# Optimization experiments

Hardware: AMD Instinct MI355X
Metric: run time of the kernel (lower is better)

The kernel has to match this reference:

```python
import jax, jax.numpy as jnp
import numpy as np

EPS = 1e-5

def _act_quant(x):
    # per-token int8 absmax quantization (BitNet b1.58)
    scale = 127.0 / jnp.clip(jnp.max(jnp.abs(x), axis=-1, keepdims=True), EPS)
    return jnp.clip(jnp.round(x * scale), -128.0, 127.0) / scale

def _weight_quant(w):
    # per-tensor ternary quantization: round(w/mean|w|) clipped to {-1,0,1}
    scale = 1.0 / jnp.clip(jnp.mean(jnp.abs(w)), EPS)
    return jnp.clip(jnp.round(w * scale), -1.0, 1.0) / scale

def _ste(x, q):
    # straight-through estimator: forward uses q, backward passes through x
    return x + jax.lax.stop_gradient(q - x)

def bitlinear(x, w):
    xq = _ste(x, _act_quant(x))
    wq = _ste(w, _weight_quant(w))
    return jnp.einsum('btd,hd->bth', xq, wq)

def setup_inputs() -> dict:
    key = jax.random.key(0)
    k1, k2, k3 = jax.random.split(key, 3)
    B, T, D, H = 4, 1024, 2048, 8192
    x = jax.random.normal(k1, (B, T, D), dtype=jnp.float32)
    w1 = jax.random.normal(k2, (H, D), dtype=jnp.float32) * 0.02
    w2 = jax.random.normal(k3, (D, H), dtype=jnp.float32) * 0.02
    return {"x": x, "w1": w1, "w2": w2}

def reference(x, w1, w2):
    h = jax.nn.relu(bitlinear(x, w1))   # [B, T, H]
    out = bitlinear(h, w2)              # [B, T, D]
    return out
```

## Files before the change

### kernel.cpp

```cpp
#include <hip/hip_runtime.h>
#include <hip/hip_bf16.h>

#define EPSF 1e-5f

typedef int v4i __attribute__((ext_vector_type(4)));
typedef short v8s __attribute__((ext_vector_type(8)));

static constexpr int BB = 4, TT = 1024, DD = 2048, HH = 8192;
static constexpr int MROWS = BB * TT;
static constexpr long long WCOUNT = (long long)DD * HH;


__device__ __forceinline__ void async_copy16(const void* g, void* l) {
  __builtin_amdgcn_global_load_lds(
      (const __attribute__((address_space(1))) unsigned int*)g,
      (__attribute__((address_space(3))) unsigned int*)l,
      16, 0, 0);
}

__device__ __forceinline__ int pack4(float a, float b, float c, float d,
                                     float scale, float lo, float hi) {
  int ia = (int)fminf(fmaxf(rintf(a * scale), lo), hi);
  int ib = (int)fminf(fmaxf(rintf(b * scale), lo), hi);
  int ic = (int)fminf(fmaxf(rintf(c * scale), lo), hi);
  int id = (int)fminf(fmaxf(rintf(d * scale), lo), hi);
  return (ia & 0xff) | ((ib & 0xff) << 8) | ((ic & 0xff) << 16) | ((id & 0xff) << 24);
}

__device__ __forceinline__ float abs4(float4 v) {
  return fmaxf(fmaxf(fabsf(v.x), fabsf(v.y)), fmaxf(fabsf(v.z), fabsf(v.w)));
}

__device__ __forceinline__ int blockMaxI256(int v) {
  #pragma unroll
  for (int off = 32; off; off >>= 1) v = max(v, __shfl_down(v, off, 64));
  __shared__ int sm[4];
  int lane = threadIdx.x & 63, wv = threadIdx.x >> 6;
  if (lane == 0) sm[wv] = v;
  __syncthreads();
  return max(max(sm[0], sm[1]), max(sm[2], sm[3]));
}

__device__ __forceinline__ void swizzle_tiles(int& mt, int& nt) {
  int Mt = gridDim.y, Nt = gridDim.x;
  int id = blockIdx.y * Nt + blockIdx.x;
  int c = id & 7, k = id >> 3;
  int pm = (Mt >= Nt) ? 4 : 2;
  int PM = Mt / pm, PN = Nt / (8 / pm);
  int pr = c % pm, pc = c / pm;
  mt = pr * PM + (k % PM);
  nt = pc * PN + (k / PM);
}


__global__ __launch_bounds__(256) void abs_sum_kernel(
    const float* __restrict__ w1, const float* __restrict__ w2,
    float* __restrict__ partials) {
  const int y = blockIdx.y, bid = blockIdx.x, t = threadIdx.x;
  const int lane = t & 63, wv = t >> 6;
  const float4* w4 = (const float4*)(y ? w2 : w1);
  const long long base = (long long)bid * 2048;
  float4 u[8];
  #pragma unroll
  for (int k = 0; k < 8; k++) u[k] = w4[base + t + k * 256];
  float s = 0.f;
  #pragma unroll
  for (int k = 0; k < 8; k++)
    s += fabsf(u[k].x) + fabsf(u[k].y) + fabsf(u[k].z) + fabsf(u[k].w);
  #pragma unroll
  for (int off = 32; off; off >>= 1) s += __shfl_down(s, off, 64);
  __shared__ float sm[4];
  if (lane == 0) sm[wv] = s;
  __syncthreads();
  if (t == 0) partials[y * 2048 + bid] = sm[0] + sm[1] + sm[2] + sm[3];
}


__global__ __launch_bounds__(256) void quant_w_kernel(
    const float* __restrict__ w1, const float* __restrict__ w2,
    const float* __restrict__ partials, float* __restrict__ meanw,
    signed char* __restrict__ q1, signed char* __restrict__ q2) {
  const int y = blockIdx.y, bid = blockIdx.x, t = threadIdx.x;
  const int lane = t & 63, wv = t >> 6;

  double d = 0.0;
  #pragma unroll
  for (int j = 0; j < 8; j++) d += (double)partials[y * 2048 + t + j * 256];
  #pragma unroll
  for (int off = 32; off; off >>= 1) d += __shfl_down(d, off, 64);
  __shared__ double smd[4];
  if (lane == 0) smd[wv] = d;
  __syncthreads();
  double sum = smd[0] + smd[1] + smd[2] + smd[3];
  float mean = fmaxf((float)(sum * (1.0 / (double)WCOUNT)), EPSF);
  if (bid == 0 && t == 0) meanw[y] = mean;
  float sc = 1.0f / mean;

  const float4* w4 = (const float4*)(y ? w2 : w1);
  int* q4 = (int*)(y ? q2 : q1);
  const long long base = (long long)bid * 2048;
  float4 u[8];
  #pragma unroll
  for (int k = 0; k < 8; k++) u[k] = w4[base + t + k * 256];
  #pragma unroll
  for (int k = 0; k < 8; k++)
    q4[base + t + k * 256] = pack4(u[k].x, u[k].y, u[k].z, u[k].w, sc, -1.f, 1.f);
}


__global__ __launch_bounds__(256) void quant_x_kernel(
    const float* __restrict__ x, signed char* __restrict__ xq,
    float* __restrict__ ascale) {
  int lane = threadIdx.x & 63, wv = threadIdx.x >> 6;
  int row = blockIdx.x * 4 + wv;
  const float4* xr = (const float4*)(x + (size_t)row * DD);
  float4 v[8];
  #pragma unroll
  for (int j = 0; j < 8; j++) v[j] = xr[lane + j * 64];
  float m = 0.f;
  #pragma unroll
  for (int j = 0; j < 8; j++) m = fmaxf(m, abs4(v[j]));
  #pragma unroll
  for (int off = 32; off; off >>= 1) m = fmaxf(m, __shfl_down(m, off, 64));
  m = __shfl(m, 0, 64);
  float am = fmaxf(m, EPSF);
  float scale = 127.0f / am;
  int* out = (int*)(xq + (size_t)row * DD);
  #pragma unroll
  for (int j = 0; j < 8; j++)
    out[lane + j * 64] = pack4(v[j].x, v[j].y, v[j].z, v[j].w, scale, -128.f, 127.f);
  if (lane == 0) ascale[row] = am / 127.0f;
}


__global__ __launch_bounds__(256) void quant_h_kernel(
    const short* __restrict__ h, signed char* __restrict__ hq,
    float* __restrict__ a2, const float* __restrict__ a1,
    const float* __restrict__ meanw) {
  int row = blockIdx.x;
  int t = threadIdx.x;
  const v8s* hr = (const v8s*)(h + (size_t)row * HH);
  v8s v[4];
  #pragma unroll
  for (int i = 0; i < 4; i++) v[i] = hr[t + i * 256];
  int mx = 0;
  #pragma unroll
  for (int i = 0; i < 4; i++)
    #pragma unroll
    for (int j = 0; j < 8; j++) mx = max(mx, (int)v[i][j]);
  int bmx = blockMaxI256(mx);
  float f = a1[row] * meanw[0];
  float maxh = (float)bmx * f;
  float am = fmaxf(maxh, EPSF);
  float scale = 127.0f / am;
  int* out = (int*)(hq + (size_t)row * HH);
  #pragma unroll
  for (int i = 0; i < 4; i++) {
    out[(t + i * 256) * 2] =
        pack4((float)v[i][0] * f, (float)v[i][1] * f, (float)v[i][2] * f,
              (float)v[i][3] * f, scale, -128.f, 127.f);
    out[(t + i * 256) * 2 + 1] =
        pack4((float)v[i][4] * f, (float)v[i][5] * f, (float)v[i][6] * f,
              (float)v[i][7] * f, scale, -128.f, 127.f);
  }
  if (t == 0) a2[row] = am / 127.0f;
}


template <int MODE, int BK>
__global__ __launch_bounds__(256) void gemm_i8_kernel(
    const signed char* __restrict__ A, const signed char* __restrict__ B,
    void* __restrict__ Cout, const float* __restrict__ ascale,
    const float* __restrict__ wmean_p, int M, int N, int K) {
  constexpr int CH = BK / 16;
  constexpr int SEGROWS = 1024 / BK;
  constexpr int SPW = BK / 32;
  __shared__ signed char As[128 * BK];
  __shared__ signed char Bs[128 * BK];

  const int t = threadIdx.x;
  const int lane = t & 63, wv = t >> 6;
  const int wm = wv >> 1, wn = wv & 1;
  int mt, nt;
  swizzle_tiles(mt, nt);
  const int m0 = mt * 128, n0 = nt * 128;
  const int q = lane >> 4;

  const signed char* aSrc[SPW];
  const signed char* bSrc[SPW];
  #pragma unroll
  for (int i = 0; i < SPW; i++) {
    int seg = wv * SPW + i;
    int r = seg * SEGROWS + lane / CH;
    int c = (lane % CH) ^ (r & (CH - 1));
    aSrc[i] = A + (size_t)(m0 + r) * K + c * 16;
    bSrc[i] = B + (size_t)(n0 + r) * K + c * 16;
  }

  v4i acc[4][4];
  #pragma unroll
  for (int i = 0; i < 4; i++)
    #pragma unroll
    for (int j = 0; j < 4; j++) {
      v4i z = {0, 0, 0, 0};
      acc[i][j] = z;
    }

  int rowA[4], rowB[4];
  #pragma unroll
  for (int i = 0; i < 4; i++) {
    rowA[i] = wm * 64 + i * 16 + (lane & 15);
    rowB[i] = wn * 64 + i * 16 + (lane & 15);
  }

  for (int k0 = 0; k0 < K; k0 += BK) {
    #pragma unroll
    for (int i = 0; i < SPW; i++) {
      async_copy16(aSrc[i] + k0, &As[(wv * SPW + i) * 1024]);
      async_copy16(bSrc[i] + k0, &Bs[(wv * SPW + i) * 1024]);
    }
    __syncthreads();
    #pragma unroll
    for (int kc = 0; kc < CH / 4; kc++) {
      v4i af[4], bf[4];
      #pragma unroll
      for (int i = 0; i < 4; i++) {
        int ca = (kc * 4 + q) ^ (rowA[i] & (CH - 1));
        af[i] = *(const v4i*)(As + rowA[i] * BK + ca * 16);
        int cb = (kc * 4 + q) ^ (rowB[i] & (CH - 1));
        bf[i] = *(const v4i*)(Bs + rowB[i] * BK + cb * 16);
      }
      #pragma unroll
      for (int i = 0; i < 4; i++)
        #pragma unroll
        for (int j = 0; j < 4; j++)
          acc[i][j] = __builtin_amdgcn_mfma_i32_16x16x64_i8(af[i], bf[j], acc[i][j], 0, 0, 0);
    }
    __syncthreads();
  }

  if constexpr (MODE == 1) {
    short* C = (short*)Cout;
    #pragma unroll
    for (int i = 0; i < 4; i++) {
      int mBase = m0 + wm * 64 + i * 16 + q * 4;
      #pragma unroll
      for (int e = 0; e < 4; e++) {
        #pragma unroll
        for (int j = 0; j < 4; j++) {
          int n = n0 + wn * 64 + j * 16 + (lane & 15);
          int r = acc[i][j][e];
          r = r < 0 ? 0 : (r > 32767 ? 32767 : r);
          C[(size_t)(mBase + e) * N + n] = (short)r;
        }
      }
    }
  } else {
    float* C = (float*)Cout;
    float wmean = wmean_p[0];
    #pragma unroll
    for (int i = 0; i < 4; i++) {
      int mBase = m0 + wm * 64 + i * 16 + q * 4;
      #pragma unroll
      for (int e = 0; e < 4; e++) {
        float f = ascale[mBase + e] * wmean;
        #pragma unroll
        for (int j = 0; j < 4; j++) {
          int n = n0 + wn * 64 + j * 16 + (lane & 15);
          C[(size_t)(mBase + e) * N + n] = (float)acc[i][j][e] * f;
        }
      }
    }
  }
}


extern "C" void kernel_launch(void* const* d_in, const int* in_sizes, int n_in,
                              void* d_out, int out_size, void* d_ws, size_t ws_size,
                              hipStream_t stream) {
  const float* x  = (const float*)d_in[0];
  const float* w1 = (const float*)d_in[1];
  const float* w2 = (const float*)d_in[2];
  float* out = (float*)d_out;

  char* ws = (char*)d_ws;
  float* meanw = (float*)ws;
  float* partials = (float*)(ws + 1024);
  float* a1 = (float*)(ws + 20480);
  float* a2 = (float*)(ws + 40960);
  signed char* w1q = (signed char*)(ws + 65536);
  signed char* w2q = w1q + (size_t)WCOUNT;
  signed char* xq  = w2q + (size_t)WCOUNT;
  signed char* hq  = xq + (size_t)MROWS * DD;
  short* h16 = (short*)(hq + (size_t)MROWS * HH);

  abs_sum_kernel<<<dim3(2048, 2), 256, 0, stream>>>(w1, w2, partials);
  quant_w_kernel<<<dim3(2048, 2), 256, 0, stream>>>(w1, w2, partials, meanw, w1q, w2q);
  quant_x_kernel<<<MROWS / 4, 256, 0, stream>>>(x, xq, a1);
  gemm_i8_kernel<1, 128><<<dim3(HH / 128, MROWS / 128), 256, 0, stream>>>(
      xq, w1q, h16, nullptr, meanw, MROWS, HH, DD);
  quant_h_kernel<<<MROWS, 256, 0, stream>>>(h16, hq, a2, a1, meanw);
  gemm_i8_kernel<0, 256><<<dim3(DD / 128, MROWS / 128), 256, 0, stream>>>(
      hq, w2q, out, a2, &meanw[1], MROWS, DD, HH);
}
```

Before: 375.2 us.

## Replace int8 GEMM with 4-slot async LDS ring pipeline and larger 512-thread tiles

```diff
diff --git a/kernel.cpp b/kernel.cpp
--- a/kernel.cpp
+++ b/kernel.cpp
@@ -16,6 +16,20 @@
       (const __attribute__((address_space(1))) unsigned int*)g,
       (__attribute__((address_space(3))) unsigned int*)l,
       16, 0, 0);
+}
+
+template <int N>
+__device__ __forceinline__ void wait_bar() {
+  if constexpr (N == 8)
+    asm volatile("s_waitcnt vmcnt(8)\n\ts_barrier" ::: "memory");
+  else if constexpr (N == 6)
+    asm volatile("s_waitcnt vmcnt(6)\n\ts_barrier" ::: "memory");
+  else if constexpr (N == 4)
+    asm volatile("s_waitcnt vmcnt(4)\n\ts_barrier" ::: "memory");
+  else if constexpr (N == 3)
+    asm volatile("s_waitcnt vmcnt(3)\n\ts_barrier" ::: "memory");
+  else
+    asm volatile("s_waitcnt vmcnt(0)\n\ts_barrier" ::: "memory");
 }
 
 __device__ __forceinline__ int pack4(float a, float b, float c, float d,
@@ -167,88 +181,125 @@
 }
 
 
-template <int MODE, int BK>
-__global__ __launch_bounds__(256) void gemm_i8_kernel(
+template <int MODE, int BM, int BN, int WM, int WN>
+__global__ __launch_bounds__(512, 2) void gemm_i8_ring(
     const signed char* __restrict__ A, const signed char* __restrict__ B,
     void* __restrict__ Cout, const float* __restrict__ ascale,
     const float* __restrict__ wmean_p, int M, int N, int K) {
-  constexpr int CH = BK / 16;
-  constexpr int SEGROWS = 1024 / BK;
-  constexpr int SPW = BK / 32;
-  __shared__ signed char As[128 * BK];
-  __shared__ signed char Bs[128 * BK];
+  static_assert(WM * WN == 8, "8 waves");
+  constexpr int WTM = BM / WM, WTN = BN / WN;
+  constexpr int MI = WTM / 16, NJ = WTN / 16;
+  constexpr int SA_W = BM / 128;
+  constexpr int SB_W = BN / 128;
+  constexpr int L = SA_W + SB_W;
+  constexpr int ABYTES = BM * 64, BBYTES = BN * 64;
+
+  __shared__ __align__(16) signed char As[4][ABYTES];
+  __shared__ __align__(16) signed char Bs[4][BBYTES];
 
   const int t = threadIdx.x;
   const int lane = t & 63, wv = t >> 6;
-  const int wm = wv >> 1, wn = wv & 1;
+  const int wm = wv / WN, wn = wv % WN;
+  const int q = lane >> 4;
+
   int mt, nt;
   swizzle_tiles(mt, nt);
-  const int m0 = mt * 128, n0 = nt * 128;
-  const int q = lane >> 4;
-
-  const signed char* aSrc[SPW];
-  const signed char* bSrc[SPW];
-  #pragma unroll
-  for (int i = 0; i < SPW; i++) {
-    int seg = wv * SPW + i;
-    int r = seg * SEGROWS + lane / CH;
-    int c = (lane % CH) ^ (r & (CH - 1));
-    aSrc[i] = A + (size_t)(m0 + r) * K + c * 16;
-    bSrc[i] = B + (size_t)(n0 + r) * K + c * 16;
-  }
-
-  v4i acc[4][4];
-  #pragma unroll
-  for (int i = 0; i < 4; i++)
-    #pragma unroll
-    for (int j = 0; j < 4; j++) {
+  const int m0 = mt * BM, n0 = nt * BN;
+
+  const signed char* aSrcP[SA_W];
+  int aDst[SA_W];
+  #pragma unroll
+  for (int i = 0; i < SA_W; i++) {
+    int seg = wv * SA_W + i;
+    int r = seg * 16 + (lane >> 2);
+    int c = (lane & 3) ^ ((r >> 1) & 3);
+    aSrcP[i] = A + (size_t)(m0 + r) * K + c * 16;
+    aDst[i] = seg * 1024;
+  }
+  const signed char* bSrcP[SB_W];
+  int bDst[SB_W];
+  #pragma unroll
+  for (int i = 0; i < SB_W; i++) {
+    int seg = wv * SB_W + i;
+    int r = seg * 16 + (lane >> 2);
+    int c = (lane & 3) ^ ((r >> 1) & 3);
+    bSrcP[i] = B + (size_t)(n0 + r) * K + c * 16;
+    bDst[i] = seg * 1024;
+  }
+
+  int aOff[MI], bOff[NJ];
+  #pragma unroll
+  for (int i = 0; i < MI; i++) {
+    int r = wm * WTM + i * 16 + (lane & 15);
+    aOff[i] = r * 64 + ((q ^ ((r >> 1) & 3)) << 4);
+  }
+  #pragma unroll
+  for (int j = 0; j < NJ; j++) {
+    int r = wn * WTN + j * 16 + (lane & 15);
+    bOff[j] = r * 64 + ((q ^ ((r >> 1) & 3)) << 4);
+  }
+
+  v4i acc[MI][NJ];
+  #pragma unroll
+  for (int i = 0; i < MI; i++)
+    #pragma unroll
+    for (int j = 0; j < NJ; j++) {
       v4i z = {0, 0, 0, 0};
       acc[i][j] = z;
     }
 
-  int rowA[4], rowB[4];
-  #pragma unroll
-  for (int i = 0; i < 4; i++) {
-    rowA[i] = wm * 64 + i * 16 + (lane & 15);
-    rowB[i] = wn * 64 + i * 16 + (lane & 15);
-  }
-
-  for (int k0 = 0; k0 < K; k0 += BK) {
-    #pragma unroll
-    for (int i = 0; i < SPW; i++) {
-      async_copy16(aSrc[i] + k0, &As[(wv * SPW + i) * 1024]);
-      async_copy16(bSrc[i] + k0, &Bs[(wv * SPW + i) * 1024]);
-    }
-    __syncthreads();
-    #pragma unroll
-    for (int kc = 0; kc < CH / 4; kc++) {
-      v4i af[4], bf[4];
+  auto stage = [&](int kt, int sl) {
+    #pragma unroll
+    for (int i = 0; i < SA_W; i++)
+      async_copy16(aSrcP[i] + (size_t)kt * 64, &As[sl][aDst[i]]);
+    #pragma unroll
+    for (int i = 0; i < SB_W; i++)
+      async_copy16(bSrcP[i] + (size_t)kt * 64, &Bs[sl][bDst[i]]);
+  };
+  auto compute = [&](int sl) {
+    const signed char* as_ = As[sl];
+    const signed char* bs_ = Bs[sl];
+    v4i af[MI], bf[NJ];
+    #pragma unroll
+    for (int i = 0; i < MI; i++) af[i] = *(const v4i*)(as_ + aOff[i]);
+    #pragma unroll
+    for (int j = 0; j < NJ; j++) bf[j] = *(const v4i*)(bs_ + bOff[j]);
+    __builtin_amdgcn_s_setprio(1);
+    #pragma unroll
+    for (int i = 0; i < MI; i++)
       #pragma unroll
-      for (int i = 0; i < 4; i++) {
-        int ca = (kc * 4 + q) ^ (rowA[i] & (CH - 1));
-        af[i] = *(const v4i*)(As + rowA[i] * BK + ca * 16);
-        int cb = (kc * 4 + q) ^ (rowB[i] & (CH - 1));
-        bf[i] = *(const v4i*)(Bs + rowB[i] * BK + cb * 16);
-      }
-      #pragma unroll
-      for (int i = 0; i < 4; i++)
-        #pragma unroll
-        for (int j = 0; j < 4; j++)
-          acc[i][j] = __builtin_amdgcn_mfma_i32_16x16x64_i8(af[i], bf[j], acc[i][j], 0, 0, 0);
-    }
-    __syncthreads();
-  }
+      for (int j = 0; j < NJ; j++)
+        acc[i][j] =
+            __builtin_amdgcn_mfma_i32_16x16x64_i8(af[i], bf[j], acc[i][j], 0, 0, 0);
+    __builtin_amdgcn_s_setprio(0);
+  };
+
+  const int NTK = K >> 6;
+  stage(0, 0);
+  stage(1, 1);
+  stage(2, 2);
+  wait_bar<2 * L>();
+  for (int kt = 0; kt < NTK - 3; ++kt) {
+    stage(kt + 3, (kt + 3) & 3);
+    compute(kt & 3);
+    wait_bar<2 * L>();
+  }
+  compute((NTK - 3) & 3);
+  wait_bar<L>();
+  compute((NTK - 2) & 3);
+  wait_bar<0>();
+  compute((NTK - 1) & 3);
 
   if constexpr (MODE == 1) {
     short* C = (short*)Cout;
     #pragma unroll
-    for (int i = 0; i < 4; i++) {
-      int mBase = m0 + wm * 64 + i * 16 + q * 4;
+    for (int i = 0; i < MI; i++) {
+      int mBase = m0 + wm * WTM + i * 16 + q * 4;
       #pragma unroll
       for (int e = 0; e < 4; e++) {
         #pragma unroll
-        for (int j = 0; j < 4; j++) {
-          int n = n0 + wn * 64 + j * 16 + (lane & 15);
+        for (int j = 0; j < NJ; j++) {
+          int n = n0 + wn * WTN + j * 16 + (lane & 15);
           int r = acc[i][j][e];
           r = r < 0 ? 0 : (r > 32767 ? 32767 : r);
           C[(size_t)(mBase + e) * N + n] = (short)r;
@@ -259,14 +310,14 @@
     float* C = (float*)Cout;
     float wmean = wmean_p[0];
     #pragma unroll
-    for (int i = 0; i < 4; i++) {
-      int mBase = m0 + wm * 64 + i * 16 + q * 4;
+    for (int i = 0; i < MI; i++) {
+      int mBase = m0 + wm * WTM + i * 16 + q * 4;
       #pragma unroll
       for (int e = 0; e < 4; e++) {
         float f = ascale[mBase + e] * wmean;
         #pragma unroll
-        for (int j = 0; j < 4; j++) {
-          int n = n0 + wn * 64 + j * 16 + (lane & 15);
+        for (int j = 0; j < NJ; j++) {
+          int n = n0 + wn * WTN + j * 16 + (lane & 15);
           C[(size_t)(mBase + e) * N + n] = (float)acc[i][j][e] * f;
         }
       }
@@ -297,9 +348,9 @@
   abs_sum_kernel<<<dim3(2048, 2), 256, 0, stream>>>(w1, w2, partials);
   quant_w_kernel<<<dim3(2048, 2), 256, 0, stream>>>(w1, w2, partials, meanw, w1q, w2q);
   quant_x_kernel<<<MROWS / 4, 256, 0, stream>>>(x, xq, a1);
-  gemm_i8_kernel<1, 128><<<dim3(HH / 128, MROWS / 128), 256, 0, stream>>>(
+  gemm_i8_ring<1, 256, 256, 2, 4><<<dim3(HH / 256, MROWS / 256), 512, 0, stream>>>(
       xq, w1q, h16, nullptr, meanw, MROWS, HH, DD);
   quant_h_kernel<<<MROWS, 256, 0, stream>>>(h16, hq, a2, a1, meanw);
-  gemm_i8_kernel<0, 256><<<dim3(DD / 128, MROWS / 128), 256, 0, stream>>>(
+  gemm_i8_ring<0, 256, 128, 4, 2><<<dim3(DD / 128, MROWS / 256), 512, 0, stream>>>(
       hq, w2q, out, a2, &meanw[1], MROWS, DD, HH);
 }
```

New measurement: 417.2 us. 11.2% more time.

## Add 256x256-tile, 4-stage pipelined int8 GEMM for first layer

Applied to the files above, without the earlier changes.

```diff
diff --git a/kernel.cpp b/kernel.cpp
--- a/kernel.cpp
+++ b/kernel.cpp
@@ -164,6 +164,131 @@
               (float)v[i][7] * f, scale, -128.f, 127.f);
   }
   if (t == 0) a2[row] = am / 127.0f;
+}
+
+
+__global__ __launch_bounds__(512, 2) void gemm1_8ph(
+    const signed char* __restrict__ A, const signed char* __restrict__ B,
+    short* __restrict__ C, int M, int N, int K) {
+  __shared__ __align__(16) signed char As[4][256 * 64];
+  __shared__ __align__(16) signed char Bs[4][256 * 64];
+
+  const int t = threadIdx.x;
+  const int lane = t & 63, wv = t >> 6;
+  const int wm = wv >> 2, wn = wv & 3;
+  const int q = lane >> 4;
+
+  int mt, nt;
+  swizzle_tiles(mt, nt);
+  const int m0 = mt * 256, n0 = nt * 256;
+
+  const signed char* aS[2];
+  const signed char* bS[2];
+  int dOf[2];
+  #pragma unroll
+  for (int j = 0; j < 2; j++) {
+    int n = t + j * 512;
+    int r = n >> 2;
+    int cg = (n & 3) ^ ((r >> 1) & 3);
+    aS[j] = A + (size_t)(m0 + r) * K + cg * 16;
+    bS[j] = B + (size_t)(n0 + r) * K + cg * 16;
+    dOf[j] = (wv * 64 + j * 512) * 16;
+  }
+
+  int aOff[8], bOff[4];
+  #pragma unroll
+  for (int i = 0; i < 8; i++) {
+    int r = wm * 128 + i * 16 + (lane & 15);
+    aOff[i] = r * 64 + ((q ^ ((r >> 1) & 3)) << 4);
+  }
+  #pragma unroll
+  for (int j = 0; j < 4; j++) {
+    int r = wn * 64 + j * 16 + (lane & 15);
+    bOff[j] = r * 64 + ((q ^ ((r >> 1) & 3)) << 4);
+  }
+
+  v4i acc[8][4];
+  #pragma unroll
+  for (int i = 0; i < 8; i++)
+    #pragma unroll
+    for (int j = 0; j < 4; j++) {
+      v4i z = {0, 0, 0, 0};
+      acc[i][j] = z;
+    }
+
+  auto stageHalf = [&](int kt, int sl, int j) {
+    async_copy16(aS[j] + (size_t)kt * 64, &As[sl][dOf[j]]);
+    async_copy16(bS[j] + (size_t)kt * 64, &Bs[sl][dOf[j]]);
+  };
+
+  const int NTK = K >> 6;
+
+  #pragma unroll
+  for (int p = 0; p < 3; p++) {
+    stageHalf(p, p, 0);
+    stageHalf(p, p, 1);
+  }
+  asm volatile("s_waitcnt vmcnt(8)\n\ts_barrier" ::: "memory");
+
+  v4i af[4], af2[4], bf[4];
+  for (int kt = 0; kt < NTK; ++kt) {
+    const int sl = kt & 3;
+    const signed char* as_ = As[sl];
+    const signed char* bs_ = Bs[sl];
+    const bool st = (kt + 3 < NTK);
+
+    #pragma unroll
+    for (int j = 0; j < 4; j++) bf[j] = *(const v4i*)(bs_ + bOff[j]);
+    #pragma unroll
+    for (int i = 0; i < 4; i++) af[i] = *(const v4i*)(as_ + aOff[i]);
+    if (st) stageHalf(kt + 3, (kt + 3) & 3, 0);
+    asm volatile("s_barrier" ::: "memory");
+    __builtin_amdgcn_s_setprio(1);
+    #pragma unroll
+    for (int i = 0; i < 4; i++)
+      #pragma unroll
+      for (int j = 0; j < 4; j++)
+        acc[i][j] =
+            __builtin_amdgcn_mfma_i32_16x16x64_i8(af[i], bf[j], acc[i][j], 0, 0, 0);
+    __builtin_amdgcn_s_setprio(0);
+    asm volatile("s_waitcnt lgkmcnt(0)\n\ts_barrier" ::: "memory");
+
+    #pragma unroll
+    for (int i = 0; i < 4; i++) af2[i] = *(const v4i*)(as_ + aOff[i + 4]);
+    if (st) stageHalf(kt + 3, (kt + 3) & 3, 1);
+    asm volatile("s_barrier" ::: "memory");
+    __builtin_amdgcn_s_setprio(1);
+    #pragma unroll
+    for (int i = 0; i < 4; i++)
+      #pragma unroll
+      for (int j = 0; j < 4; j++)
+        acc[i + 4][j] =
+            __builtin_amdgcn_mfma_i32_16x16x64_i8(af2[i], bf[j], acc[i + 4][j], 0, 0, 0);
+    __builtin_amdgcn_s_setprio(0);
+    if (kt < NTK - 3)
+      asm volatile("s_waitcnt vmcnt(8) lgkmcnt(0)\n\ts_barrier" ::: "memory");
+    else if (kt == NTK - 3)
+      asm volatile("s_waitcnt vmcnt(4) lgkmcnt(0)\n\ts_barrier" ::: "memory");
+    else if (kt == NTK - 2)
+      asm volatile("s_waitcnt vmcnt(0) lgkmcnt(0)\n\ts_barrier" ::: "memory");
+    else
+      asm volatile("s_waitcnt lgkmcnt(0)" ::: "memory");
+  }
+
+  #pragma unroll
+  for (int i = 0; i < 8; i++) {
+    int mBase = m0 + wm * 128 + i * 16 + q * 4;
+    #pragma unroll
+    for (int e = 0; e < 4; e++) {
+      #pragma unroll
+      for (int j = 0; j < 4; j++) {
+        int n = n0 + wn * 64 + j * 16 + (lane & 15);
+        int r = acc[i][j][e];
+        r = r < 0 ? 0 : (r > 32767 ? 32767 : r);
+        C[(size_t)(mBase + e) * N + n] = (short)r;
+      }
+    }
+  }
 }
 
 
@@ -297,8 +422,8 @@
   abs_sum_kernel<<<dim3(2048, 2), 256, 0, stream>>>(w1, w2, partials);
   quant_w_kernel<<<dim3(2048, 2), 256, 0, stream>>>(w1, w2, partials, meanw, w1q, w2q);
   quant_x_kernel<<<MROWS / 4, 256, 0, stream>>>(x, xq, a1);
-  gemm_i8_kernel<1, 128><<<dim3(HH / 128, MROWS / 128), 256, 0, stream>>>(
-      xq, w1q, h16, nullptr, meanw, MROWS, HH, DD);
+  gemm1_8ph<<<dim3(HH / 256, MROWS / 256), 512, 0, stream>>>(
+      xq, w1q, h16, MROWS, HH, DD);
   quant_h_kernel<<<MROWS, 256, 0, stream>>>(h16, hq, a2, a1, meanw);
   gemm_i8_kernel<0, 256><<<dim3(DD / 128, MROWS / 128), 256, 0, stream>>>(
       hq, w2q, out, a2, &meanw[1], MROWS, DD, HH);
```

After: 374.7 us. About the same (-0.1%).
